# Kernel optimization log

Hardware: AMD Instinct MI355X
Metric: run time of the kernel (lower is better)

The kernel has to match this reference:

```python
import jax, jax.numpy as jnp
import numpy as np

N_REQ = 100000
N_CODE = 100000
C_IN = 256
C_OUT = 256
HEADS = 8
DIM = C_OUT // HEADS  # 32
E = 500000
E_LAB = 200000
NEG_SLOPE = 0.2
BN_EPS = 1e-5


def setup_inputs() -> dict:
    key = jax.random.key(0)
    ks = jax.random.split(key, 20)
    s = 0.05
    return {
        "x_req": jax.random.normal(ks[0], (N_REQ, C_IN), jnp.float32),
        "x_code": jax.random.normal(ks[1], (N_CODE, C_IN), jnp.float32),
        "edge_index_rc": jax.random.randint(ks[2], (2, E), 0, N_CODE),  # req -> code
        "edge_index_cr": jax.random.randint(ks[3], (2, E), 0, N_REQ),   # code -> req
        "edge_label_index": jax.random.randint(ks[4], (2, E_LAB), 0, N_REQ),
        # per-node-type projections
        "W_req": jax.random.normal(ks[5], (C_OUT, C_IN), jnp.float32) * s,
        "b_req": jnp.zeros((C_OUT,), jnp.float32),
        "W_code": jax.random.normal(ks[6], (C_OUT, C_IN), jnp.float32) * s,
        "b_code": jnp.zeros((C_OUT,), jnp.float32),
        # per-edge-type attention vectors [heads, dim]
        "att_src_rc": jax.random.normal(ks[7], (HEADS, DIM), jnp.float32) * s,
        "att_dst_rc": jax.random.normal(ks[8], (HEADS, DIM), jnp.float32) * s,
        "att_src_cr": jax.random.normal(ks[9], (HEADS, DIM), jnp.float32) * s,
        "att_dst_cr": jax.random.normal(ks[10], (HEADS, DIM), jnp.float32) * s,
        # semantic-level attention
        "k_W": jax.random.normal(ks[11], (C_OUT, C_OUT), jnp.float32) * s,
        "k_b": jnp.zeros((C_OUT,), jnp.float32),
        "q": jax.random.normal(ks[12], (C_OUT,), jnp.float32) * s,
        # BatchNorm1d affine params (shared bn1 applied to each node type)
        "gamma": jnp.ones((C_OUT,), jnp.float32),
        "beta": jnp.zeros((C_OUT,), jnp.float32),
    }


def _segment_softmax(logits, seg, num_segments):
    # logits: [E, H], softmax over edges sharing the same destination node
    m = jax.ops.segment_max(logits, seg, num_segments=num_segments)
    m = jnp.where(jnp.isfinite(m), m, 0.0)
    e = jnp.exp(logits - m[seg])
    s = jax.ops.segment_sum(e, seg, num_segments=num_segments)
    return e / (s[seg] + 1e-16)


def _han_edge(x_src, x_dst, edge_index, att_s, att_d, n_dst):
    # x_src: [N_src, H, D], x_dst: [N_dst, H, D]
    a_s = jnp.einsum('nhd,hd->nh', x_src, att_s)
    a_d = jnp.einsum('nhd,hd->nh', x_dst, att_d)
    src, dst = edge_index[0], edge_index[1]
    alpha = jax.nn.leaky_relu(a_s[src] + a_d[dst], NEG_SLOPE)   # [E, H]
    alpha = _segment_softmax(alpha, dst, n_dst)
    msg = x_src[src] * alpha[:, :, None]                        # [E, H, D]
    out = jax.ops.segment_sum(msg, dst, num_segments=n_dst)     # [N_dst, H, D]
    return jax.nn.relu(out.reshape(n_dst, HEADS * DIM))


def _group(outs, q, k_W, k_b):
    # semantic-level attention over metapaths (PyG HANConv group)
    stacked = jnp.stack(outs)                                   # [M, N, C]
    k = jnp.tanh(stacked @ k_W.T + k_b).mean(axis=1)            # [M, C]
    attn = jax.nn.softmax((q * k).sum(-1))                      # [M]
    return jnp.einsum('m,mnc->nc', attn, stacked)


def _batchnorm(x, gamma, beta):
    mu = x.mean(axis=0)
    var = x.var(axis=0)  # biased, as torch BN uses for normalization
    return (x - mu) * jax.lax.rsqrt(var + BN_EPS) * gamma + beta


def reference(x_req, x_code, edge_index_rc, edge_index_cr, edge_label_index,
              W_req, b_req, W_code, b_code,
              att_src_rc, att_dst_rc, att_src_cr, att_dst_cr,
              k_W, k_b, q, gamma, beta):
    # node-type projections -> [N, H, D]
    h_req = (x_req @ W_req.T + b_req).reshape(-1, HEADS, DIM)
    h_code = (x_code @ W_code.T + b_code).reshape(-1, HEADS, DIM)

    # per-edge-type GAT-style propagation
    out_code = _han_edge(h_req, h_code, edge_index_rc, att_src_rc, att_dst_rc, N_CODE)
    out_req = _han_edge(h_code, h_req, edge_index_cr, att_src_cr, att_dst_cr, N_REQ)

    # semantic attention fusion (one metapath per node type here)
    z_req = _group([out_req], q, k_W, k_b)
    z_code = _group([out_code], q, k_W, k_b)

    # shared BatchNorm1d applied per node type (training-mode batch stats)
    z_req = _batchnorm(z_req, gamma, beta)
    z_code = _batchnorm(z_code, gamma, beta)

    # edge dot-product classifier
    feat_req = z_req[edge_label_index[0]]
    feat_code = z_code[edge_label_index[1]]
    return jax.nn.sigmoid((feat_req * feat_code).sum(axis=-1))
```

## Files before the change

kernel.cpp:

```cpp
#include <hip/hip_runtime.h>
#include <cstdint>
#include <cstddef>

namespace {

constexpr int kN    = 100000;
constexpr int kNpad = 100096;
constexpr int kE    = 500000;
constexpr int kEL   = 200000;
constexpr int kC    = 256;
constexpr int kH    = 8;
constexpr float kNegSlope = 0.2f;
constexpr float kBnEps    = 1e-5f;

typedef float    f32x4  __attribute__((ext_vector_type(4)));
typedef __bf16   bf16x8 __attribute__((ext_vector_type(8)));
typedef _Float16 h4     __attribute__((ext_vector_type(4)));

__device__ inline unsigned short bf16_rtn(float x) {
  unsigned u = __builtin_bit_cast(unsigned, x);
  unsigned r = (u + 0x7fffu + ((u >> 16) & 1u)) >> 16;
  return (unsigned short)r;
}
__device__ inline float bf16_f(unsigned short h) {
  unsigned u = ((unsigned)h) << 16;
  return __builtin_bit_cast(float, u);
}

__device__ inline void async_copy16(unsigned short* lds, const unsigned short* g) {
  __builtin_amdgcn_global_load_lds(
      (const __attribute__((address_space(1))) unsigned int*)g,
      (__attribute__((address_space(3))) unsigned int*)lds, 16, 0, 0);
}

__global__ void zero2_kernel(int* __restrict__ p0, int* __restrict__ p1, int n) {
  const int i = blockIdx.x * 256 + threadIdx.x;
  if (i < n) {
    p0[i] = 0;
    p1[i] = 0;
  }
}

__global__ __launch_bounds__(256) void cvt_kernel(
    const float* __restrict__ in, unsigned short* __restrict__ hi,
    unsigned short* __restrict__ lo, int n4) {
  const int i = blockIdx.x * 256 + threadIdx.x;
  if (i >= n4) return;
  const float4 v = ((const float4*)in)[i];
  const unsigned short h0 = bf16_rtn(v.x), h1 = bf16_rtn(v.y),
                       h2 = bf16_rtn(v.z), h3 = bf16_rtn(v.w);
  ((ushort4*)hi)[i] = make_ushort4(h0, h1, h2, h3);
  ((ushort4*)lo)[i] = make_ushort4(bf16_rtn(v.x - bf16_f(h0)),
                                   bf16_rtn(v.y - bf16_f(h1)),
                                   bf16_rtn(v.z - bf16_f(h2)),
                                   bf16_rtn(v.w - bf16_f(h3)));
}

__global__ __launch_bounds__(256) void gemm_fused_kernel(
    const float* __restrict__ X0, const float* __restrict__ X1,
    const unsigned short* __restrict__ Whi0, const unsigned short* __restrict__ Wlo0,
    const unsigned short* __restrict__ Whi1, const unsigned short* __restrict__ Wlo1,
    const float* __restrict__ bias0, const float* __restrict__ bias1,
    _Float16* __restrict__ H0, _Float16* __restrict__ H1) {
  __shared__ unsigned short sAhi[128 * 32];
  __shared__ unsigned short sAlo[128 * 32];
  __shared__ unsigned short sBhi[128 * 32];
  __shared__ unsigned short sBlo[128 * 32];

  const bool t1 = (blockIdx.z != 0);
  const float* __restrict__ X            = t1 ? X1 : X0;
  const unsigned short* __restrict__ Whi = t1 ? Whi1 : Whi0;
  const unsigned short* __restrict__ Wlo = t1 ? Wlo1 : Wlo0;
  const float* __restrict__ bias         = t1 ? bias1 : bias0;
  _Float16* __restrict__ H               = t1 ? H1 : H0;

  const int tid  = threadIdx.x;
  const int m0   = blockIdx.y * 128;
  const int n0   = blockIdx.x * 128;
  const int w    = tid >> 6, lane = tid & 63, l16 = lane & 15, quad = lane >> 4;
  const int wm   = (w >> 1) * 64, wn = (w & 1) * 64;

  const int arow = w * 32 + (lane >> 3);
  const int acol = (lane & 7) * 4;
  const size_t bbase = (size_t)(n0 + (lane >> 2)) * kC + (lane & 3) * 8;

  f32x4 acc[4][4] = {};

  for (int kt = 0; kt < kC / 32; ++kt) {
    const int k0 = kt * 32;
    __syncthreads();
    async_copy16(sBhi + (2 * w) * 512,     Whi + bbase + (size_t)(2 * w) * 16 * kC + k0);
    async_copy16(sBhi + (2 * w + 1) * 512, Whi + bbase + (size_t)(2 * w + 1) * 16 * kC + k0);
    async_copy16(sBlo + (2 * w) * 512,     Wlo + bbase + (size_t)(2 * w) * 16 * kC + k0);
    async_copy16(sBlo + (2 * w + 1) * 512, Wlo + bbase + (size_t)(2 * w + 1) * 16 * kC + k0);
    f32x4 av[4];
#pragma unroll
    for (int j = 0; j < 4; ++j) {
      const int grow = min(m0 + arow + j * 8, kN - 1);
      av[j] = *(const f32x4*)&X[(size_t)grow * kC + k0 + acol];
    }
#pragma unroll
    for (int j = 0; j < 4; ++j) {
      const int row = arow + j * 8;
      ushort4 hi, lo;
      hi.x = bf16_rtn(av[j][0]); lo.x = bf16_rtn(av[j][0] - bf16_f(hi.x));
      hi.y = bf16_rtn(av[j][1]); lo.y = bf16_rtn(av[j][1] - bf16_f(hi.y));
      hi.z = bf16_rtn(av[j][2]); lo.z = bf16_rtn(av[j][2] - bf16_f(hi.z));
      hi.w = bf16_rtn(av[j][3]); lo.w = bf16_rtn(av[j][3] - bf16_f(hi.w));
      *(ushort4*)&sAhi[row * 32 + acol] = hi;
      *(ushort4*)&sAlo[row * 32 + acol] = lo;
    }
    __syncthreads();

    bf16x8 ah[4], al[4], bh[4], bl[4];
#pragma unroll
    for (int mi = 0; mi < 4; ++mi) {
      const int row = wm + mi * 16 + l16;
      ah[mi] = *(const bf16x8*)&sAhi[row * 32 + quad * 8];
      al[mi] = *(const bf16x8*)&sAlo[row * 32 + quad * 8];
    }
#pragma unroll
    for (int ni = 0; ni < 4; ++ni) {
      const int row = wn + ni * 16 + l16;
      bh[ni] = *(const bf16x8*)&sBhi[row * 32 + quad * 8];
      bl[ni] = *(const bf16x8*)&sBlo[row * 32 + quad * 8];
    }
#pragma unroll
    for (int mi = 0; mi < 4; ++mi)
#pragma unroll
      for (int ni = 0; ni < 4; ++ni) {
        acc[mi][ni] = __builtin_amdgcn_mfma_f32_16x16x32_bf16(ah[mi], bh[ni], acc[mi][ni], 0, 0, 0);
        acc[mi][ni] = __builtin_amdgcn_mfma_f32_16x16x32_bf16(ah[mi], bl[ni], acc[mi][ni], 0, 0, 0);
        acc[mi][ni] = __builtin_amdgcn_mfma_f32_16x16x32_bf16(al[mi], bh[ni], acc[mi][ni], 0, 0, 0);
      }
  }

#pragma unroll
  for (int ni = 0; ni < 4; ++ni) {
    const int col = n0 + wn + ni * 16 + l16;
    const float bc = bias[col];
#pragma unroll
    for (int mi = 0; mi < 4; ++mi) {
      const int gm0 = m0 + wm + mi * 16 + quad * 4;
#pragma unroll
      for (int r = 0; r < 4; ++r) {
        const int gm = gm0 + r;
        if (gm < kN) H[(size_t)gm * kC + col] = (_Float16)(acc[mi][ni][r] + bc);
      }
    }
  }
}

__global__ __launch_bounds__(256) void avec_kernel(
    const _Float16* __restrict__ h, const float* __restrict__ attA,
    const float* __restrict__ attB, float* __restrict__ outA,
    float* __restrict__ outB, int N) {
  const int n = blockIdx.x * 4 + (threadIdx.x >> 6);
  if (n >= N) return;
  const int L = threadIdx.x & 63;
  const h4 hv = *(const h4*)&h[(size_t)n * kC + 4 * L];
  const float4 a = *(const float4*)&attA[4 * L];
  const float4 b = *(const float4*)&attB[4 * L];
  const float hx = (float)hv.x, hy = (float)hv.y, hz = (float)hv.z, hw = (float)hv.w;
  float pa = hx * a.x + hy * a.y + hz * a.z + hw * a.w;
  float pb = hx * b.x + hy * b.y + hz * b.z + hw * b.w;
  for (int m = 1; m < 8; m <<= 1) {
    pa += __shfl_xor(pa, m);
    pb += __shfl_xor(pb, m);
  }
  if ((L & 7) == 0) {
    outA[n * kH + (L >> 3)] = pa;
    outB[n * kH + (L >> 3)] = pb;
  }
}

__global__ void count_kernel(const int* __restrict__ dst, int E, int* __restrict__ cnt) {
  const int e = blockIdx.x * 256 + threadIdx.x;
  if (e < E) atomicAdd(&cnt[dst[e]], 1);
}

__global__ void scan1_kernel(const int* __restrict__ cnt, int N,
                             int* __restrict__ off, int* __restrict__ part) {
  __shared__ int s[256];
  const int t = threadIdx.x;
  const int i = blockIdx.x * 256 + t;
  const int v = (i < N) ? cnt[i] : 0;
  s[t] = v;
  __syncthreads();
  for (int o = 1; o < 256; o <<= 1) {
    const int x = (t >= o) ? s[t - o] : 0;
    __syncthreads();
    s[t] += x;
    __syncthreads();
  }
  if (i < N) off[i] = s[t] - v;
  if (t == 255) part[blockIdx.x] = s[255];
}

__global__ void scan2_kernel(int* __restrict__ part, int NB) {
  __shared__ int s[512];
  const int t = threadIdx.x;
  const int v = (t < NB) ? part[t] : 0;
  s[t] = v;
  __syncthreads();
  for (int o = 1; o < 512; o <<= 1) {
    const int x = (t >= o) ? s[t - o] : 0;
    __syncthreads();
    s[t] += x;
    __syncthreads();
  }
  if (t < NB) part[t] = s[t] - v;
}

__global__ void scan3_kernel(int* __restrict__ off, int* __restrict__ cur,
                             const int* __restrict__ part, int N) {
  const int i = blockIdx.x * 256 + threadIdx.x;
  if (i < N) {
    const int v = off[i] + part[blockIdx.x];
    off[i] = v;
    cur[i] = v;
  }
}

__global__ void scatter_kernel(const int* __restrict__ dst,
                               const int* __restrict__ srcv, int E,
                               int* __restrict__ cur, int* __restrict__ perm) {
  const int e = blockIdx.x * 256 + threadIdx.x;
  if (e < E) {
    const int p = atomicAdd(&cur[dst[e]], 1);
    perm[p] = srcv[e];
  }
}

__global__ __launch_bounds__(256) void aggregate2_kernel(
    const _Float16* __restrict__ h0, const float* __restrict__ aS0,
    const float* __restrict__ aD0, const int* __restrict__ srcs0,
    const int* __restrict__ off0, const int* __restrict__ cnt0,
    float* __restrict__ out0,
    const _Float16* __restrict__ h1, const float* __restrict__ aS1,
    const float* __restrict__ aD1, const int* __restrict__ srcs1,
    const int* __restrict__ off1, const int* __restrict__ cnt1,
    float* __restrict__ out1) {
  const int d = blockIdx.x * 4 + (threadIdx.x >> 6);
  if (d >= kN) return;
  const bool dir1 = (blockIdx.y != 0);
  const _Float16* __restrict__ hsrc = dir1 ? h1 : h0;
  const float* __restrict__ aS   = dir1 ? aS1 : aS0;
  const float* __restrict__ aD   = dir1 ? aD1 : aD0;
  const int* __restrict__ srcs   = dir1 ? srcs1 : srcs0;
  const int* __restrict__ off    = dir1 ? off1 : off0;
  const int* __restrict__ cnt    = dir1 ? cnt1 : cnt0;
  float* __restrict__ out        = dir1 ? out1 : out0;

  const int L  = threadIdx.x & 63;
  const int hd = L >> 3;
  const float ad = aD[d * kH + hd];
  const int o = off[d], c = cnt[d];
  float4 acc = make_float4(0.f, 0.f, 0.f, 0.f);
  float se = 0.f;
  int i = 0;
  for (; i + 4 <= c; i += 4) {
    const int s0 = srcs[o + i], s1 = srcs[o + i + 1];
    const int s2 = srcs[o + i + 2], s3 = srcs[o + i + 3];
    const float a0 = aS[s0 * kH + hd], a1 = aS[s1 * kH + hd];
    const float a2 = aS[s2 * kH + hd], a3 = aS[s3 * kH + hd];
    const h4 v0 = *(const h4*)&hsrc[(size_t)s0 * kC + 4 * L];
    const h4 v1 = *(const h4*)&hsrc[(size_t)s1 * kC + 4 * L];
    const h4 v2 = *(const h4*)&hsrc[(size_t)s2 * kC + 4 * L];
    const h4 v3 = *(const h4*)&hsrc[(size_t)s3 * kC + 4 * L];
    float t0 = a0 + ad; t0 = t0 > 0.f ? t0 : kNegSlope * t0;
    float t1 = a1 + ad; t1 = t1 > 0.f ? t1 : kNegSlope * t1;
    float t2 = a2 + ad; t2 = t2 > 0.f ? t2 : kNegSlope * t2;
    float t3 = a3 + ad; t3 = t3 > 0.f ? t3 : kNegSlope * t3;
    const float w0 = __expf(t0), w1 = __expf(t1);
    const float w2 = __expf(t2), w3 = __expf(t3);
    se += (w0 + w1) + (w2 + w3);
    acc.x += w0 * (float)v0.x + w1 * (float)v1.x + w2 * (float)v2.x + w3 * (float)v3.x;
    acc.y += w0 * (float)v0.y + w1 * (float)v1.y + w2 * (float)v2.y + w3 * (float)v3.y;
    acc.z += w0 * (float)v0.z + w1 * (float)v1.z + w2 * (float)v2.z + w3 * (float)v3.z;
    acc.w += w0 * (float)v0.w + w1 * (float)v1.w + w2 * (float)v2.w + w3 * (float)v3.w;
  }
  for (; i < c; ++i) {
    const int s = srcs[o + i];
    float t = aS[s * kH + hd] + ad;
    t = t > 0.f ? t : kNegSlope * t;
    const float wgt = __expf(t);
    se += wgt;
    const h4 hv = *(const h4*)&hsrc[(size_t)s * kC + 4 * L];
    acc.x += wgt * (float)hv.x;
    acc.y += wgt * (float)hv.y;
    acc.z += wgt * (float)hv.z;
    acc.w += wgt * (float)hv.w;
  }
  const float inv = 1.f / (se + 1e-16f);
  float4 r;
  r.x = fmaxf(acc.x * inv, 0.f);
  r.y = fmaxf(acc.y * inv, 0.f);
  r.z = fmaxf(acc.z * inv, 0.f);
  r.w = fmaxf(acc.w * inv, 0.f);
  *(float4*)&out[(size_t)d * kC + 4 * L] = r;
}

constexpr int kBnB = 512;
__global__ __launch_bounds__(256) void bn_stats_kernel(
    const float* __restrict__ xr, const float* __restrict__ xc,
    float* __restrict__ part) {
  __shared__ f32x4 red[2][4][64];
  const float* __restrict__ x = blockIdx.y ? xc : xr;
  const int t = threadIdx.x, w = t >> 6, L = t & 63;
  const int rowsPer = (kN + kBnB - 1) / kBnB;
  const int r0 = blockIdx.x * rowsPer;
  const int r1 = min(r0 + rowsPer, kN);
  f32x4 s0 = {0.f, 0.f, 0.f, 0.f}, q0 = {0.f, 0.f, 0.f, 0.f};
  f32x4 s1 = {0.f, 0.f, 0.f, 0.f}, q1 = {0.f, 0.f, 0.f, 0.f};
  f32x4 s2 = {0.f, 0.f, 0.f, 0.f}, q2 = {0.f, 0.f, 0.f, 0.f};
  f32x4 s3 = {0.f, 0.f, 0.f, 0.f}, q3 = {0.f, 0.f, 0.f, 0.f};
  int r = r0 + w;
  for (; r + 12 < r1; r += 16) {
    const f32x4 v0 = *(const f32x4*)&x[(size_t)(r)      * kC + 4 * L];
    const f32x4 v1 = *(const f32x4*)&x[(size_t)(r + 4)  * kC + 4 * L];
    const f32x4 v2 = *(const f32x4*)&x[(size_t)(r + 8)  * kC + 4 * L];
    const f32x4 v3 = *(const f32x4*)&x[(size_t)(r + 12) * kC + 4 * L];
    s0 += v0; q0 += v0 * v0;
    s1 += v1; q1 += v1 * v1;
    s2 += v2; q2 += v2 * v2;
    s3 += v3; q3 += v3 * v3;
  }
  for (; r < r1; r += 4) {
    const f32x4 v = *(const f32x4*)&x[(size_t)r * kC + 4 * L];
    s0 += v; q0 += v * v;
  }
  const f32x4 s = (s0 + s1) + (s2 + s3);
  const f32x4 q = (q0 + q1) + (q2 + q3);
  red[0][w][L] = s;
  red[1][w][L] = q;
  __syncthreads();
  if (w == 0) {
    const f32x4 ts = red[0][0][L] + red[0][1][L] + red[0][2][L] + red[0][3][L];
    const f32x4 t2 = red[1][0][L] + red[1][1][L] + red[1][2][L] + red[1][3][L];
    float* dst = part + ((size_t)blockIdx.y * kBnB + blockIdx.x) * 512;
    *(f32x4*)&dst[4 * L]       = ts;
    *(f32x4*)&dst[256 + 4 * L] = t2;
  }
}

__global__ __launch_bounds__(256) void bn_final_kernel(
    const float* __restrict__ part, const float* __restrict__ gamma,
    const float* __restrict__ beta, float* __restrict__ sb) {
  const int c = threadIdx.x;
  const int t = blockIdx.x;
  const float* __restrict__ p0 = part + (size_t)t * kBnB * 512;
  float s = 0.f, q = 0.f;
#pragma unroll 4
  for (int b = 0; b < kBnB; ++b) {
    s += p0[b * 512 + c];
    q += p0[b * 512 + 256 + c];
  }
  const float mu  = s * (1.f / kN);
  const float var = q * (1.f / kN) - mu * mu;
  const float sc  = gamma[c] * rsqrtf(var + kBnEps);
  sb[t * 512 + c]       = sc;
  sb[t * 512 + 256 + c] = beta[c] - mu * sc;
}

__global__ __launch_bounds__(256) void classify_kernel(
    const float* __restrict__ zr, const float* __restrict__ zc,
    const int* __restrict__ ei, const int* __restrict__ ej,
    const float* __restrict__ sb, float* __restrict__ y, int EL) {
  const int e = blockIdx.x * 4 + (threadIdx.x >> 6);
  if (e >= EL) return;
  const int L = threadIdx.x & 63;
  const int i = ei[e], j = ej[e];
  const float4 a  = *(const float4*)&zr[(size_t)i * kC + 4 * L];
  const float4 b  = *(const float4*)&zc[(size_t)j * kC + 4 * L];
  const float4 sr = *(const float4*)&sb[4 * L];
  const float4 br = *(const float4*)&sb[256 + 4 * L];
  const float4 sc = *(const float4*)&sb[512 + 4 * L];
  const float4 bc = *(const float4*)&sb[768 + 4 * L];
  float p = (a.x * sr.x + br.x) * (b.x * sc.x + bc.x) +
            (a.y * sr.y + br.y) * (b.y * sc.y + bc.y) +
            (a.z * sr.z + br.z) * (b.z * sc.z + bc.z) +
            (a.w * sr.w + br.w) * (b.w * sc.w + bc.w);
  for (int m = 1; m < 64; m <<= 1) p += __shfl_xor(p, m);
  if (L == 0) y[e] = 1.f / (1.f + __expf(-p));
}

}

extern "C" void kernel_launch(void* const* d_in, const int* in_sizes, int n_in,
                              void* d_out, int out_size, void* d_ws, size_t ws_size,
                              hipStream_t stream) {
  (void)in_sizes; (void)n_in; (void)out_size; (void)ws_size;
  const float* x_req      = (const float*)d_in[0];
  const float* x_code     = (const float*)d_in[1];
  const int*   ei_rc      = (const int*)d_in[2];
  const int*   ei_cr      = (const int*)d_in[3];
  const int*   el         = (const int*)d_in[4];
  const float* W_req      = (const float*)d_in[5];
  const float* b_req      = (const float*)d_in[6];
  const float* W_code     = (const float*)d_in[7];
  const float* b_code     = (const float*)d_in[8];
  const float* att_src_rc = (const float*)d_in[9];
  const float* att_dst_rc = (const float*)d_in[10];
  const float* att_src_cr = (const float*)d_in[11];
  const float* att_dst_cr = (const float*)d_in[12];
  const float* gamma      = (const float*)d_in[16];
  const float* beta       = (const float*)d_in[17];
  float* y = (float*)d_out;

  char* p = (char*)d_ws;
  auto alloc = [&](size_t bytes) {
    char* r = p;
    p += (bytes + 1023) & ~(size_t)1023;
    return r;
  };
  unsigned short* Xhi = (unsigned short*)alloc((size_t)kNpad * kC * 2);
  unsigned short* Xlo = (unsigned short*)alloc((size_t)kNpad * kC * 2);
  (void)Xlo;
  float* out_code = (float*)Xhi;
  _Float16* h_req  = (_Float16*)alloc((size_t)kN * kC * 2);
  _Float16* h_code = (_Float16*)alloc((size_t)kN * kC * 2);
  float* out_req   = (float*)alloc((size_t)kN * kC * 4);
  unsigned short* Whi_r = (unsigned short*)alloc((size_t)kC * kC * 2);
  unsigned short* Wlo_r = (unsigned short*)alloc((size_t)kC * kC * 2);
  unsigned short* Whi_c = (unsigned short*)alloc((size_t)kC * kC * 2);
  unsigned short* Wlo_c = (unsigned short*)alloc((size_t)kC * kC * 2);
  float* a_src_rc = (float*)alloc((size_t)kN * kH * 4);
  float* a_dst_rc = (float*)alloc((size_t)kN * kH * 4);
  float* a_src_cr = (float*)alloc((size_t)kN * kH * 4);
  float* a_dst_cr = (float*)alloc((size_t)kN * kH * 4);
  int* cnt_rc  = (int*)alloc((size_t)kN * 4);
  int* off_rc  = (int*)alloc((size_t)kN * 4);
  int* cur_rc  = (int*)alloc((size_t)kN * 4);
  int* perm_rc = (int*)alloc((size_t)kE * 4);
  int* cnt_cr  = (int*)alloc((size_t)kN * 4);
  int* off_cr  = (int*)alloc((size_t)kN * 4);
  int* cur_cr  = (int*)alloc((size_t)kN * 4);
  int* perm_cr = (int*)alloc((size_t)kE * 4);
  int*   part  = (int*)alloc(512 * 4);
  float* bnpart = (float*)a_src_rc;
  float* sb     = (float*)a_src_cr;

  const int nScanB = (kN + 255) / 256;
  const int nW4    = kC * kC / 4;

  zero2_kernel<<<nScanB, 256, 0, stream>>>(cnt_rc, cnt_cr, kN);

  cvt_kernel<<<(nW4 + 255) / 256, 256, 0, stream>>>(W_req, Whi_r, Wlo_r, nW4);
  cvt_kernel<<<(nW4 + 255) / 256, 256, 0, stream>>>(W_code, Whi_c, Wlo_c, nW4);

  gemm_fused_kernel<<<dim3(kC / 128, kNpad / 128, 2), 256, 0, stream>>>(
      x_req, x_code, Whi_r, Wlo_r, Whi_c, Wlo_c, b_req, b_code, h_req, h_code);

  avec_kernel<<<(kN + 3) / 4, 256, 0, stream>>>(h_req, att_src_rc, att_dst_cr,
                                                a_src_rc, a_dst_cr, kN);
  avec_kernel<<<(kN + 3) / 4, 256, 0, stream>>>(h_code, att_src_cr, att_dst_rc,
                                                a_src_cr, a_dst_rc, kN);

  const int* src_rc = ei_rc;
  const int* dst_rc = ei_rc + kE;
  const int* src_cr = ei_cr;
  const int* dst_cr = ei_cr + kE;
  count_kernel<<<(kE + 255) / 256, 256, 0, stream>>>(dst_rc, kE, cnt_rc);
  count_kernel<<<(kE + 255) / 256, 256, 0, stream>>>(dst_cr, kE, cnt_cr);
  scan1_kernel<<<nScanB, 256, 0, stream>>>(cnt_rc, kN, off_rc, part);
  scan2_kernel<<<1, 512, 0, stream>>>(part, nScanB);
  scan3_kernel<<<nScanB, 256, 0, stream>>>(off_rc, cur_rc, part, kN);
  scan1_kernel<<<nScanB, 256, 0, stream>>>(cnt_cr, kN, off_cr, part);
  scan2_kernel<<<1, 512, 0, stream>>>(part, nScanB);
  scan3_kernel<<<nScanB, 256, 0, stream>>>(off_cr, cur_cr, part, kN);
  scatter_kernel<<<(kE + 255) / 256, 256, 0, stream>>>(dst_rc, src_rc, kE, cur_rc, perm_rc);
  scatter_kernel<<<(kE + 255) / 256, 256, 0, stream>>>(dst_cr, src_cr, kE, cur_cr, perm_cr);

  aggregate2_kernel<<<dim3((kN + 3) / 4, 2), 256, 0, stream>>>(
      h_req, a_src_rc, a_dst_rc, perm_rc, off_rc, cnt_rc, out_code,
      h_code, a_src_cr, a_dst_cr, perm_cr, off_cr, cnt_cr, out_req);

  bn_stats_kernel<<<dim3(kBnB, 2), 256, 0, stream>>>(out_req, out_code, bnpart);
  bn_final_kernel<<<2, 256, 0, stream>>>(bnpart, gamma, beta, sb);

  classify_kernel<<<(kEL + 3) / 4, 256, 0, stream>>>(
      out_req, out_code, el, el + kEL, sb, y, kEL);
}
```

Before: 752.2 us.

## Double-buffer shared-memory tiles in fused projection GEMM to overlap loads with MFMA

Doubles the LDS tiles for the A and B operands and restructures the k-loop into a software pipeline. The next tile's weight async copies and activation global loads are issued before the MFMAs on the current tile, and the bf16 split of A is written afterward. This hides global memory latency behind compute and removes one barrier per iteration. It doubles LDS use per block, which may lower occupancy, and keeps the prefetched A values in registers.

```diff
diff --git a/kernel.cpp b/kernel.cpp
--- a/kernel.cpp
+++ b/kernel.cpp
@@ -62,10 +62,10 @@
     const unsigned short* __restrict__ Whi1, const unsigned short* __restrict__ Wlo1,
     const float* __restrict__ bias0, const float* __restrict__ bias1,
     _Float16* __restrict__ H0, _Float16* __restrict__ H1) {
-  __shared__ unsigned short sAhi[128 * 32];
-  __shared__ unsigned short sAlo[128 * 32];
-  __shared__ unsigned short sBhi[128 * 32];
-  __shared__ unsigned short sBlo[128 * 32];
+  __shared__ unsigned short sAhi[2][128 * 32];
+  __shared__ unsigned short sAlo[2][128 * 32];
+  __shared__ unsigned short sBhi[2][128 * 32];
+  __shared__ unsigned short sBlo[2][128 * 32];
 
   const bool t1 = (blockIdx.z != 0);
   const float* __restrict__ X            = t1 ? X1 : X0;
@@ -85,20 +85,23 @@
   const size_t bbase = (size_t)(n0 + (lane >> 2)) * kC + (lane & 3) * 8;
 
   f32x4 acc[4][4] = {};
-
-  for (int kt = 0; kt < kC / 32; ++kt) {
-    const int k0 = kt * 32;
-    __syncthreads();
-    async_copy16(sBhi + (2 * w) * 512,     Whi + bbase + (size_t)(2 * w) * 16 * kC + k0);
-    async_copy16(sBhi + (2 * w + 1) * 512, Whi + bbase + (size_t)(2 * w + 1) * 16 * kC + k0);
-    async_copy16(sBlo + (2 * w) * 512,     Wlo + bbase + (size_t)(2 * w) * 16 * kC + k0);
-    async_copy16(sBlo + (2 * w + 1) * 512, Wlo + bbase + (size_t)(2 * w + 1) * 16 * kC + k0);
-    f32x4 av[4];
+  f32x4 av[4];
+
+  auto loadA = [&](int kt) {
 #pragma unroll
     for (int j = 0; j < 4; ++j) {
       const int grow = min(m0 + arow + j * 8, kN - 1);
-      av[j] = *(const f32x4*)&X[(size_t)grow * kC + k0 + acol];
+      av[j] = *(const f32x4*)&X[(size_t)grow * kC + kt * 32 + acol];
     }
+  };
+  auto stageB = [&](int kt, int buf) {
+    const int k0 = kt * 32;
+    async_copy16(sBhi[buf] + (2 * w) * 512,     Whi + bbase + (size_t)(2 * w) * 16 * kC + k0);
+    async_copy16(sBhi[buf] + (2 * w + 1) * 512, Whi + bbase + (size_t)(2 * w + 1) * 16 * kC + k0);
+    async_copy16(sBlo[buf] + (2 * w) * 512,     Wlo + bbase + (size_t)(2 * w) * 16 * kC + k0);
+    async_copy16(sBlo[buf] + (2 * w + 1) * 512, Wlo + bbase + (size_t)(2 * w + 1) * 16 * kC + k0);
+  };
+  auto writeA = [&](int buf) {
 #pragma unroll
     for (int j = 0; j < 4; ++j) {
       const int row = arow + j * 8;
@@ -107,23 +110,35 @@
       hi.y = bf16_rtn(av[j][1]); lo.y = bf16_rtn(av[j][1] - bf16_f(hi.y));
       hi.z = bf16_rtn(av[j][2]); lo.z = bf16_rtn(av[j][2] - bf16_f(hi.z));
       hi.w = bf16_rtn(av[j][3]); lo.w = bf16_rtn(av[j][3] - bf16_f(hi.w));
-      *(ushort4*)&sAhi[row * 32 + acol] = hi;
-      *(ushort4*)&sAlo[row * 32 + acol] = lo;
+      *(ushort4*)&sAhi[buf][row * 32 + acol] = hi;
+      *(ushort4*)&sAlo[buf][row * 32 + acol] = lo;
     }
-    __syncthreads();
+  };
+
+  loadA(0);
+  stageB(0, 0);
+  writeA(0);
+  __syncthreads();
+
+  for (int kt = 0; kt < kC / 32; ++kt) {
+    const int cur = kt & 1, nxt = cur ^ 1;
+    if (kt + 1 < kC / 32) {
+      stageB(kt + 1, nxt);
+      loadA(kt + 1);
+    }
 
     bf16x8 ah[4], al[4], bh[4], bl[4];
 #pragma unroll
     for (int mi = 0; mi < 4; ++mi) {
       const int row = wm + mi * 16 + l16;
-      ah[mi] = *(const bf16x8*)&sAhi[row * 32 + quad * 8];
-      al[mi] = *(const bf16x8*)&sAlo[row * 32 + quad * 8];
+      ah[mi] = *(const bf16x8*)&sAhi[cur][row * 32 + quad * 8];
+      al[mi] = *(const bf16x8*)&sAlo[cur][row * 32 + quad * 8];
     }
 #pragma unroll
     for (int ni = 0; ni < 4; ++ni) {
       const int row = wn + ni * 16 + l16;
-      bh[ni] = *(const bf16x8*)&sBhi[row * 32 + quad * 8];
-      bl[ni] = *(const bf16x8*)&sBlo[row * 32 + quad * 8];
+      bh[ni] = *(const bf16x8*)&sBhi[cur][row * 32 + quad * 8];
+      bl[ni] = *(const bf16x8*)&sBlo[cur][row * 32 + quad * 8];
     }
 #pragma unroll
     for (int mi = 0; mi < 4; ++mi)
@@ -133,6 +148,9 @@
         acc[mi][ni] = __builtin_amdgcn_mfma_f32_16x16x32_bf16(ah[mi], bl[ni], acc[mi][ni], 0, 0, 0);
         acc[mi][ni] = __builtin_amdgcn_mfma_f32_16x16x32_bf16(al[mi], bh[ni], acc[mi][ni], 0, 0, 0);
       }
+
+    if (kt + 1 < kC / 32) writeA(nxt);
+    __syncthreads();
   }
 
 #pragma unroll
```

After: 773.3 us. 1.03x slower.

## Load GEMM operands directly from global into MFMA registers, dropping LDS staging

Applied to the files above, without the earlier changes.

The projection GEMM no longer stages A and B tiles through shared memory with barriers. Each lane now loads its MFMA fragments straight from global memory, converting X to hi/lo bf16 in registers. This removes LDS traffic and two __syncthreads per k-step. In exchange, A rows are reloaded and converted by both column-warps and B is reloaded by both row-warps without sharing, which relies on L1/L2 and uses less coalesced access.

```diff
diff --git a/kernel.cpp b/kernel.cpp
--- a/kernel.cpp
+++ b/kernel.cpp
@@ -25,12 +25,6 @@
 __device__ inline float bf16_f(unsigned short h) {
   unsigned u = ((unsigned)h) << 16;
   return __builtin_bit_cast(float, u);
-}
-
-__device__ inline void async_copy16(unsigned short* lds, const unsigned short* g) {
-  __builtin_amdgcn_global_load_lds(
-      (const __attribute__((address_space(1))) unsigned int*)g,
-      (__attribute__((address_space(3))) unsigned int*)lds, 16, 0, 0);
 }
 
 __global__ void zero2_kernel(int* __restrict__ p0, int* __restrict__ p1, int n) {
@@ -62,11 +56,6 @@
     const unsigned short* __restrict__ Whi1, const unsigned short* __restrict__ Wlo1,
     const float* __restrict__ bias0, const float* __restrict__ bias1,
     _Float16* __restrict__ H0, _Float16* __restrict__ H1) {
-  __shared__ unsigned short sAhi[128 * 32];
-  __shared__ unsigned short sAlo[128 * 32];
-  __shared__ unsigned short sBhi[128 * 32];
-  __shared__ unsigned short sBlo[128 * 32];
-
   const bool t1 = (blockIdx.z != 0);
   const float* __restrict__ X            = t1 ? X1 : X0;
   const unsigned short* __restrict__ Whi = t1 ? Whi1 : Whi0;
@@ -80,51 +69,40 @@
   const int w    = tid >> 6, lane = tid & 63, l16 = lane & 15, quad = lane >> 4;
   const int wm   = (w >> 1) * 64, wn = (w & 1) * 64;
 
-  const int arow = w * 32 + (lane >> 3);
-  const int acol = (lane & 7) * 4;
-  const size_t bbase = (size_t)(n0 + (lane >> 2)) * kC + (lane & 3) * 8;
+  int arow[4], brow[4];
+#pragma unroll
+  for (int mi = 0; mi < 4; ++mi) arow[mi] = min(m0 + wm + mi * 16 + l16, kN - 1);
+#pragma unroll
+  for (int ni = 0; ni < 4; ++ni) brow[ni] = wn + ni * 16 + l16;
 
   f32x4 acc[4][4] = {};
 
   for (int kt = 0; kt < kC / 32; ++kt) {
-    const int k0 = kt * 32;
-    __syncthreads();
-    async_copy16(sBhi + (2 * w) * 512,     Whi + bbase + (size_t)(2 * w) * 16 * kC + k0);
-    async_copy16(sBhi + (2 * w + 1) * 512, Whi + bbase + (size_t)(2 * w + 1) * 16 * kC + k0);
-    async_copy16(sBlo + (2 * w) * 512,     Wlo + bbase + (size_t)(2 * w) * 16 * kC + k0);
-    async_copy16(sBlo + (2 * w + 1) * 512, Wlo + bbase + (size_t)(2 * w + 1) * 16 * kC + k0);
-    f32x4 av[4];
-#pragma unroll
-    for (int j = 0; j < 4; ++j) {
-      const int grow = min(m0 + arow + j * 8, kN - 1);
-      av[j] = *(const f32x4*)&X[(size_t)grow * kC + k0 + acol];
+    const int k0 = kt * 32 + quad * 8;
+
+    bf16x8 ah[4], al[4], bh[4], bl[4];
+#pragma unroll
+    for (int mi = 0; mi < 4; ++mi) {
+      const float* xp = &X[(size_t)arow[mi] * kC + k0];
+      const f32x4 x0 = *(const f32x4*)xp;
+      const f32x4 x1 = *(const f32x4*)(xp + 4);
+#pragma unroll
+      for (int j = 0; j < 4; ++j) {
+        const __bf16 h0 = (__bf16)x0[j];
+        const __bf16 h1 = (__bf16)x1[j];
+        ah[mi][j]     = h0;
+        ah[mi][j + 4] = h1;
+        al[mi][j]     = (__bf16)(x0[j] - (float)h0);
+        al[mi][j + 4] = (__bf16)(x1[j] - (float)h1);
+      }
     }
 #pragma unroll
-    for (int j = 0; j < 4; ++j) {
-      const int row = arow + j * 8;
-      ushort4 hi, lo;
-      hi.x = bf16_rtn(av[j][0]); lo.x = bf16_rtn(av[j][0] - bf16_f(hi.x));
-      hi.y = bf16_rtn(av[j][1]); lo.y = bf16_rtn(av[j][1] - bf16_f(hi.y));
-      hi.z = bf16_rtn(av[j][2]); lo.z = bf16_rtn(av[j][2] - bf16_f(hi.z));
-      hi.w = bf16_rtn(av[j][3]); lo.w = bf16_rtn(av[j][3] - bf16_f(hi.w));
-      *(ushort4*)&sAhi[row * 32 + acol] = hi;
-      *(ushort4*)&sAlo[row * 32 + acol] = lo;
+    for (int ni = 0; ni < 4; ++ni) {
+      const size_t boff = (size_t)(n0 + brow[ni]) * kC + k0;
+      bh[ni] = *(const bf16x8*)&Whi[boff];
+      bl[ni] = *(const bf16x8*)&Wlo[boff];
     }
-    __syncthreads();
-
-    bf16x8 ah[4], al[4], bh[4], bl[4];
-#pragma unroll
-    for (int mi = 0; mi < 4; ++mi) {
-      const int row = wm + mi * 16 + l16;
-      ah[mi] = *(const bf16x8*)&sAhi[row * 32 + quad * 8];
-      al[mi] = *(const bf16x8*)&sAlo[row * 32 + quad * 8];
-    }
-#pragma unroll
-    for (int ni = 0; ni < 4; ++ni) {
-      const int row = wn + ni * 16 + l16;
-      bh[ni] = *(const bf16x8*)&sBhi[row * 32 + quad * 8];
-      bl[ni] = *(const bf16x8*)&sBlo[row * 32 + quad * 8];
-    }
+
 #pragma unroll
     for (int mi = 0; mi < 4; ++mi)
 #pragma unroll
```

Result: slower. 852.8 us (+13.4%).
